# Kernel optimization log

Measured on AMD Instinct MI355X. Metric: run time of the kernel, lower is better.

The kernel has to match this reference:

```python
import jax, jax.numpy as jnp
import numpy as np

B, S, D, NH, K = 4, 2048, 768, 4, 4
DH = D // NH
EPS = 1e-5


def setup_inputs() -> dict:
    key = jax.random.key(0)
    ks = jax.random.split(key, 10)
    sc = 0.02
    return {
        "x": jax.random.normal(ks[0], (B, S, D), jnp.float32),
        "conv_kernel": jax.random.normal(ks[1], (K, D), jnp.float32) * sc,
        "conv_bias": jnp.zeros((D,), jnp.float32),
        "Wi": jax.random.normal(ks[2], (NH, DH, DH), jnp.float32) * sc,
        "Wf": jax.random.normal(ks[3], (NH, DH, DH), jnp.float32) * sc,
        "Wz": jax.random.normal(ks[4], (NH, DH, DH), jnp.float32) * sc,
        "Wo": jax.random.normal(ks[5], (NH, DH, DH), jnp.float32) * sc,
        "R": jax.random.normal(ks[6], (4, NH, DH, DH), jnp.float32) * sc,
        "cell_bias": jnp.zeros((4, D), jnp.float32),
        "gn_scale": jnp.ones((NH, DH), jnp.float32),
    }


def reference(x, conv_kernel, conv_bias, Wi, Wf, Wz, Wo, R, cell_bias, gn_scale):
    b, s, d = x.shape
    nh, dh, _ = Wi.shape
    k = conv_kernel.shape[0]

    # causal depthwise conv1d + swish
    xc = jax.lax.conv_general_dilated(
        x, conv_kernel[:, None, :], (1,), [(k - 1, 0)],
        dimension_numbers=("NWC", "WIO", "NWC"), feature_group_count=d,
    ) + conv_bias
    x_conv = jax.nn.swish(xc)

    # headwise (block-diagonal) gate projections, no bias
    def headwise(v, W):
        return jnp.einsum("bshd,hde->bshe", v.reshape(b, s, nh, dh), W).reshape(b, s, d)

    i_in = headwise(x_conv, Wi)
    f_in = headwise(x_conv, Wf)
    z_in = headwise(x, Wz)
    o_in = headwise(x, Wo)

    g = jnp.stack([i_in, f_in, z_in, o_in], axis=0).transpose(2, 0, 1, 3)  # (S,4,B,D)

    zeros = jnp.zeros((b, d), x.dtype)
    carry0 = (zeros, zeros, zeros, zeros)  # h, c, n, m

    def step(carry, gt):
        h, c, n, m = carry
        rec = jnp.einsum("bhd,ghde->gbhe", h.reshape(b, nh, dh), R).reshape(4, b, d)
        pre = gt + rec + cell_bias[:, None, :]
        it, ft, zt, ot = pre[0], pre[1], pre[2], pre[3]
        # stabilized exponential gating
        m_new = jnp.maximum(ft + m, it)
        iact = jnp.exp(it - m_new)
        fact = jnp.exp(ft + m - m_new)
        c_new = fact * c + iact * jnp.tanh(zt)
        n_new = fact * n + iact
        h_new = jax.nn.sigmoid(ot) * c_new / n_new
        return (h_new, c_new, n_new, m_new), h_new

    _, ys = jax.lax.scan(step, carry0, g)  # (S,B,D)

    # (B, NH, S, DH) head layout for multi-head layernorm
    y = ys.transpose(1, 0, 2).reshape(b, s, nh, dh).transpose(0, 2, 1, 3)
    mu = y.mean(-1, keepdims=True)
    var = y.var(-1, keepdims=True)
    yn = (y - mu) * jax.lax.rsqrt(var + EPS) * gn_scale[None, :, None, :]
    return yn.transpose(0, 2, 1, 3).reshape(b, s, d)
```

## Files before the change

### kernel.cpp

```cpp
#include <hip/hip_runtime.h>

#define B_  4
#define S_  2048
#define D_  768
#define NH_ 4
#define DH_ 192

typedef short  s8v __attribute__((ext_vector_type(8)));
typedef float  f4v __attribute__((ext_vector_type(4)));
typedef unsigned short ushort_t;

static __device__ __forceinline__ ushort_t f2bf(float f) {
    union { float f; unsigned u; } v; v.f = f;
    unsigned r = v.u + 0x7fffu + ((v.u >> 16) & 1u);
    return (ushort_t)(r >> 16);
}
static __device__ __forceinline__ float bf2f(ushort_t b) {
    union { unsigned u; float f; } v; v.u = ((unsigned)b) << 16;
    return v.f;
}
static __device__ __forceinline__ f4v mfma16(s8v a, s8v b, f4v c) {
    return __builtin_amdgcn_mfma_f32_16x16x32_bf16(a, b, c, 0, 0, 0);
}

__global__ void conv_kernel(const float* __restrict__ x, const float* __restrict__ ck,
                            const float* __restrict__ cb,
                            ushort_t* __restrict__ xconv, ushort_t* __restrict__ xb) {
    int idx = blockIdx.x * blockDim.x + threadIdx.x;
    const int nd4 = D_ / 4;
    int d4 = idx % nd4;
    int bs = idx / nd4;
    int s = bs % S_;
    int b = bs / S_;
    int d = d4 * 4;

    float4 acc = *(const float4*)(cb + d);
    float4 xcur = make_float4(0.f, 0.f, 0.f, 0.f);
#pragma unroll
    for (int k = 0; k < 4; ++k) {
        int sk = s - 3 + k;
        float4 xv = make_float4(0.f, 0.f, 0.f, 0.f);
        if (sk >= 0) xv = *(const float4*)(x + ((size_t)(b * S_ + sk) * D_ + d));
        if (k == 3) xcur = xv;
        float4 kv = *(const float4*)(ck + (size_t)k * D_ + d);
        acc.x += xv.x * kv.x; acc.y += xv.y * kv.y;
        acc.z += xv.z * kv.z; acc.w += xv.w * kv.w;
    }
    float c0 = acc.x / (1.f + __expf(-acc.x));
    float c1 = acc.y / (1.f + __expf(-acc.y));
    float c2 = acc.z / (1.f + __expf(-acc.z));
    float c3 = acc.w / (1.f + __expf(-acc.w));

    size_t base = (size_t)bs * D_ + d;
    ushort4 pc; pc.x = f2bf(c0); pc.y = f2bf(c1); pc.z = f2bf(c2); pc.w = f2bf(c3);
    *(ushort4*)(xconv + base) = pc;
    ushort4 px; px.x = f2bf(xcur.x); px.y = f2bf(xcur.y); px.z = f2bf(xcur.z); px.w = f2bf(xcur.w);
    *(ushort4*)(xb + base) = px;
}

__launch_bounds__(768)
__global__ void gates_kernel(const ushort_t* __restrict__ xconv, const ushort_t* __restrict__ xb,
                             const float* __restrict__ Wi, const float* __restrict__ Wf,
                             const float* __restrict__ Wz, const float* __restrict__ Wo,
                             const float* __restrict__ cbias, ushort_t* __restrict__ G) {
    int sb = blockIdx.x, h = blockIdx.y, p = blockIdx.z;
    const ushort_t* X = (p == 0) ? xconv : xb;
    const float* W0 = (p == 0) ? Wi : Wz;
    const float* W1 = (p == 0) ? Wf : Wo;
    int g0 = 2 * p, g1 = 2 * p + 1;

    int tid = threadIdx.x;
    int lane = tid & 63;
    int w = tid >> 6;

    int col = w * 16 + (lane & 15);
    int kq0 = (lane >> 4) * 8;

    s8v B0[6], B1[6];
#pragma unroll
    for (int kt = 0; kt < 6; ++kt) {
        const float* w0p = W0 + ((size_t)(h * DH_ + kt * 32 + kq0)) * DH_ + col;
        const float* w1p = W1 + ((size_t)(h * DH_ + kt * 32 + kq0)) * DH_ + col;
        s8v f0, f1;
#pragma unroll
        for (int j = 0; j < 8; ++j) {
            f0[j] = (short)f2bf(w0p[(size_t)j * DH_]);
            f1[j] = (short)f2bf(w1p[(size_t)j * DH_]);
        }
        B0[kt] = f0; B1[kt] = f1;
    }
    float bias0 = cbias[(size_t)g0 * D_ + h * DH_ + col];
    float bias1 = cbias[(size_t)g1 * D_ + h * DH_ + col];

    int b_l = lane & 3;
    int ds_l = (lane >> 2) & 3;

    for (int mt = 0; mt < 16; ++mt) {
        int s = sb * 64 + mt * 4 + ds_l;
        const ushort_t* ap = X + ((size_t)(b_l * S_ + s) * D_ + h * DH_ + kq0);
        s8v A[6];
#pragma unroll
        for (int kt = 0; kt < 6; ++kt) A[kt] = *(const s8v*)(ap + kt * 32);
        f4v a0 = {0.f, 0.f, 0.f, 0.f}, a1 = {0.f, 0.f, 0.f, 0.f};
#pragma unroll
        for (int kt = 0; kt < 6; ++kt) {
            a0 = mfma16(A[kt], B0[kt], a0);
            a1 = mfma16(A[kt], B1[kt], a1);
        }
        int sro = sb * 64 + mt * 4 + (lane >> 4);
        size_t base0 = ((size_t)(sro * NH_ + h) * 4 + g0) * (4 * DH_);
        size_t base1 = ((size_t)(sro * NH_ + h) * 4 + g1) * (4 * DH_);
#pragma unroll
        for (int r = 0; r < 4; ++r) {
            G[base0 + r * DH_ + col] = f2bf(a0[r] + bias0);
            G[base1 + r * DH_ + col] = f2bf(a1[r] + bias1);
        }
    }
}

__launch_bounds__(768)
__global__ void recur_kernel(const ushort_t* __restrict__ G, const float* __restrict__ Rw,
                             ushort_t* __restrict__ ys) {
    const int h = blockIdx.x;
    const int tid = threadIdx.x;
    const int lane = tid & 63;
    const int w = tid >> 6;

    __shared__ ushort_t h_lds[4 * 208];
    __shared__ f4v rec_lds[768];

    s8v Bf[4][6];
    {
        int col = w * 16 + (lane & 15);
        int kq0 = (lane >> 4) * 8;
#pragma unroll
        for (int g = 0; g < 4; ++g)
#pragma unroll
            for (int kt = 0; kt < 6; ++kt) {
                const float* rp = Rw + ((size_t)((g * NH_ + h) * DH_ + kt * 32 + kq0)) * DH_ + col;
                s8v f;
#pragma unroll
                for (int j = 0; j < 8; ++j) f[j] = (short)f2bf(rp[(size_t)j * DH_]);
                Bf[g][kt] = f;
            }
    }

    for (int i = tid; i < 4 * 208; i += 768) h_lds[i] = 0;

    float m_st = 0.f, c_st = 0.f, n_st = 0.f;
    const int b_idx = tid / DH_;
    const int e_idx = tid % DH_;
    const int arow = lane & 3;
    const int kq = (lane >> 4) * 8;

    ushort_t gi_n, gf_n, gz_n, go_n;
    {
        const ushort_t* gp = G + ((size_t)(0 * NH_ + h) * 4) * (4 * DH_) + tid;
        gi_n = gp[0]; gf_n = gp[768]; gz_n = gp[2 * 768]; go_n = gp[3 * 768];
    }

    __syncthreads();

    for (int s = 0; s < S_; ++s) {
        ushort_t gi = gi_n, gf = gf_n, gz = gz_n, go = go_n;
        {
            int sn = (s + 1 < S_) ? (s + 1) : s;
            const ushort_t* gp = G + ((size_t)(sn * NH_ + h) * 4) * (4 * DH_) + tid;
            gi_n = gp[0]; gf_n = gp[768]; gz_n = gp[2 * 768]; go_n = gp[3 * 768];
        }

        s8v A[6];
#pragma unroll
        for (int kt = 0; kt < 6; ++kt)
            A[kt] = *(const s8v*)&h_lds[arow * 208 + kt * 32 + kq];

        f4v acc[4];
#pragma unroll
        for (int g = 0; g < 4; ++g) { acc[g][0] = 0.f; acc[g][1] = 0.f; acc[g][2] = 0.f; acc[g][3] = 0.f; }
#pragma unroll
        for (int g = 0; g < 4; ++g)
#pragma unroll
            for (int kt = 0; kt < 6; ++kt)
                acc[g] = mfma16(A[kt], Bf[g][kt], acc[g]);

        if (lane < 16) {
            int e = w * 16 + lane;
#pragma unroll
            for (int bb = 0; bb < 4; ++bb) {
                f4v v;
                v[0] = acc[0][bb]; v[1] = acc[1][bb]; v[2] = acc[2][bb]; v[3] = acc[3][bb];
                rec_lds[bb * DH_ + e] = v;
            }
        }
        __syncthreads();

        f4v r = rec_lds[tid];
        float it = r[0] + bf2f(gi);
        float ft = r[1] + bf2f(gf);
        float zt = r[2] + bf2f(gz);
        float ot = r[3] + bf2f(go);

        float mn = fmaxf(ft + m_st, it);
        float ia = __expf(it - mn);
        float fa = __expf(ft + m_st - mn);
        float ez = __expf(2.f * zt);
        float th = 1.f - 2.f / (ez + 1.f);
        float cn = fa * c_st + ia * th;
        float nn = fa * n_st + ia;
        float sg = 1.f / (1.f + __expf(-ot));
        float hn = sg * cn / nn;
        m_st = mn; c_st = cn; n_st = nn;

        ushort_t hb = f2bf(hn);
        __syncthreads();
        h_lds[b_idx * 208 + e_idx] = hb;
        ys[(size_t)(s * NH_ + h) * (4 * DH_) + tid] = hb;
        __syncthreads();
    }
}

__global__ void ln_kernel(const ushort_t* __restrict__ ys, const float* __restrict__ gn,
                          float* __restrict__ out) {
    int gw = (blockIdx.x * blockDim.x + threadIdx.x) >> 6;
    int lane = threadIdx.x & 63;
    int b = gw & 3;
    int h = (gw >> 2) & 3;
    int s = gw >> 4;

    const ushort_t* yp = ys + (size_t)gw * DH_;
    float v0 = bf2f(yp[lane]);
    float v1 = bf2f(yp[lane + 64]);
    float v2 = bf2f(yp[lane + 128]);
    float sum = v0 + v1 + v2;
    float sq  = v0 * v0 + v1 * v1 + v2 * v2;
#pragma unroll
    for (int off = 32; off > 0; off >>= 1) {
        sum += __shfl_xor(sum, off, 64);
        sq  += __shfl_xor(sq,  off, 64);
    }
    float mu  = sum * (1.f / 192.f);
    float var = sq * (1.f / 192.f) - mu * mu;
    float rs  = rsqrtf(var + 1e-5f);

    float* op = out + (size_t)(b * S_ + s) * D_ + h * DH_;
    const float* gp = gn + h * DH_;
    op[lane]       = (v0 - mu) * rs * gp[lane];
    op[lane + 64]  = (v1 - mu) * rs * gp[lane + 64];
    op[lane + 128] = (v2 - mu) * rs * gp[lane + 128];
}

extern "C" void kernel_launch(void* const* d_in, const int* in_sizes, int n_in,
                              void* d_out, int out_size, void* d_ws, size_t ws_size,
                              hipStream_t stream) {
    const float* x     = (const float*)d_in[0];
    const float* ck    = (const float*)d_in[1];
    const float* cb    = (const float*)d_in[2];
    const float* Wi    = (const float*)d_in[3];
    const float* Wf    = (const float*)d_in[4];
    const float* Wz    = (const float*)d_in[5];
    const float* Wo    = (const float*)d_in[6];
    const float* Rw    = (const float*)d_in[7];
    const float* cbias = (const float*)d_in[8];
    const float* gn    = (const float*)d_in[9];
    float* out = (float*)d_out;

    const size_t nBSD = (size_t)B_ * S_ * D_;
    ushort_t* xconv = (ushort_t*)d_ws;
    ushort_t* xb    = xconv + nBSD;
    ushort_t* G     = xb + nBSD;
    ushort_t* ys    = G + (size_t)S_ * NH_ * 4 * B_ * DH_;

    conv_kernel<<<dim3(B_ * S_ * D_ / 4 / 256), dim3(256), 0, stream>>>(x, ck, cb, xconv, xb);
    gates_kernel<<<dim3(32, NH_, 2), dim3(768), 0, stream>>>(xconv, xb, Wi, Wf, Wz, Wo, cbias, G);
    recur_kernel<<<dim3(NH_), dim3(768), 0, stream>>>(G, Rw, ys);
    ln_kernel<<<dim3(8192), dim3(256), 0, stream>>>(ys, gn, out);
}
```

Before: 2.531 ms.

## Restructure recurrence to use MFMA output directly with double-buffered h and one barrier

After: 2.077 ms. -17.9%, faster.

```diff
diff --git a/kernel.cpp b/kernel.cpp
--- a/kernel.cpp
+++ b/kernel.cpp
@@ -108,12 +108,13 @@
             a1 = mfma16(A[kt], B1[kt], a1);
         }
         int sro = sb * 64 + mt * 4 + (lane >> 4);
-        size_t base0 = ((size_t)(sro * NH_ + h) * 4 + g0) * (4 * DH_);
-        size_t base1 = ((size_t)(sro * NH_ + h) * 4 + g1) * (4 * DH_);
 #pragma unroll
         for (int r = 0; r < 4; ++r) {
-            G[base0 + r * DH_ + col] = f2bf(a0[r] + bias0);
-            G[base1 + r * DH_ + col] = f2bf(a1[r] + bias1);
+            size_t idx = (((size_t)(sro * NH_ + h) * B_ + r) * DH_ + col) * 4;
+            ushort2 pr;
+            pr.x = f2bf(a0[r] + bias0);
+            pr.y = f2bf(a1[r] + bias1);
+            *(ushort2*)(G + idx + 2 * p) = pr;
         }
     }
 }
@@ -126,8 +127,7 @@
     const int lane = tid & 63;
     const int w = tid >> 6;
 
-    __shared__ ushort_t h_lds[4 * 208];
-    __shared__ f4v rec_lds[768];
+    __shared__ ushort_t h_lds[2 * 4 * 208];
 
     s8v Bf[4][6];
     {
@@ -145,76 +145,67 @@
             }
     }
 
-    for (int i = tid; i < 4 * 208; i += 768) h_lds[i] = 0;
+    for (int i = tid; i < 2 * 4 * 208; i += 768) h_lds[i] = 0;
+
+    const int b_id = lane >> 4;
+    const int e_id = w * 16 + (lane & 15);
+    const int a_off = ((lane & 15) >> 2) * 208 + (lane >> 4) * 8;
+    const int hw_off = b_id * 208 + e_id;
 
     float m_st = 0.f, c_st = 0.f, n_st = 0.f;
-    const int b_idx = tid / DH_;
-    const int e_idx = tid % DH_;
-    const int arow = lane & 3;
-    const int kq = (lane >> 4) * 8;
-
-    ushort_t gi_n, gf_n, gz_n, go_n;
-    {
-        const ushort_t* gp = G + ((size_t)(0 * NH_ + h) * 4) * (4 * DH_) + tid;
-        gi_n = gp[0]; gf_n = gp[768]; gz_n = gp[2 * 768]; go_n = gp[3 * 768];
-    }
+    const float LOG2E = 1.44269504088896f;
+
+    const int gstride = NH_ * B_ * DH_ * 4;
+    const ushort_t* gp = G + (((size_t)h * B_ + b_id) * DH_ + e_id) * 4;
+    ushort4 gv_n = *(const ushort4*)gp;
+
+    ushort_t* yp = ys + ((size_t)h * B_ + b_id) * DH_ + e_id;
 
     __syncthreads();
 
     for (int s = 0; s < S_; ++s) {
-        ushort_t gi = gi_n, gf = gf_n, gz = gz_n, go = go_n;
-        {
-            int sn = (s + 1 < S_) ? (s + 1) : s;
-            const ushort_t* gp = G + ((size_t)(sn * NH_ + h) * 4) * (4 * DH_) + tid;
-            gi_n = gp[0]; gf_n = gp[768]; gz_n = gp[2 * 768]; go_n = gp[3 * 768];
-        }
+        ushort4 gv = gv_n;
+        if (s + 1 < S_) gp += gstride;
+        gv_n = *(const ushort4*)gp;
+
+        const int p = s & 1;
+        const ushort_t* abuf = h_lds + p * 832 + a_off;
 
         s8v A[6];
 #pragma unroll
         for (int kt = 0; kt < 6; ++kt)
-            A[kt] = *(const s8v*)&h_lds[arow * 208 + kt * 32 + kq];
+            A[kt] = *(const s8v*)(abuf + kt * 32);
 
         f4v acc[4];
 #pragma unroll
         for (int g = 0; g < 4; ++g) { acc[g][0] = 0.f; acc[g][1] = 0.f; acc[g][2] = 0.f; acc[g][3] = 0.f; }
 #pragma unroll
-        for (int g = 0; g < 4; ++g)
-#pragma unroll
-            for (int kt = 0; kt < 6; ++kt)
+        for (int kt = 0; kt < 6; ++kt)
+#pragma unroll
+            for (int g = 0; g < 4; ++g)
                 acc[g] = mfma16(A[kt], Bf[g][kt], acc[g]);
 
-        if (lane < 16) {
-            int e = w * 16 + lane;
-#pragma unroll
-            for (int bb = 0; bb < 4; ++bb) {
-                f4v v;
-                v[0] = acc[0][bb]; v[1] = acc[1][bb]; v[2] = acc[2][bb]; v[3] = acc[3][bb];
-                rec_lds[bb * DH_ + e] = v;
-            }
-        }
-        __syncthreads();
-
-        f4v r = rec_lds[tid];
-        float it = r[0] + bf2f(gi);
-        float ft = r[1] + bf2f(gf);
-        float zt = r[2] + bf2f(gz);
-        float ot = r[3] + bf2f(go);
-
-        float mn = fmaxf(ft + m_st, it);
-        float ia = __expf(it - mn);
-        float fa = __expf(ft + m_st - mn);
-        float ez = __expf(2.f * zt);
-        float th = 1.f - 2.f / (ez + 1.f);
+        float it = acc[0][0] + bf2f(gv.x);
+        float ft = acc[1][0] + bf2f(gv.y);
+        float zt = acc[2][0] + bf2f(gv.z);
+        float ot = acc[3][0] + bf2f(gv.w);
+
+        float fm = ft + m_st;
+        float mn = fmaxf(fm, it);
+        float ia = __builtin_amdgcn_exp2f((it - mn) * LOG2E);
+        float fa = __builtin_amdgcn_exp2f((fm - mn) * LOG2E);
+        float ez = __builtin_amdgcn_exp2f(zt * (2.f * LOG2E));
+        float th = 1.f - 2.f * __builtin_amdgcn_rcpf(ez + 1.f);
         float cn = fa * c_st + ia * th;
         float nn = fa * n_st + ia;
-        float sg = 1.f / (1.f + __expf(-ot));
-        float hn = sg * cn / nn;
+        float sg = __builtin_amdgcn_rcpf(1.f + __builtin_amdgcn_exp2f(-ot * LOG2E));
+        float hn = sg * cn * __builtin_amdgcn_rcpf(nn);
         m_st = mn; c_st = cn; n_st = nn;
 
         ushort_t hb = f2bf(hn);
-        __syncthreads();
-        h_lds[b_idx * 208 + e_idx] = hb;
-        ys[(size_t)(s * NH_ + h) * (4 * DH_) + tid] = hb;
+        h_lds[(1 - p) * 832 + hw_off] = hb;
+        *yp = hb;
+        yp += NH_ * B_ * DH_;
         __syncthreads();
     }
 }
```
